# Kernel optimization log

Measured on AMD Instinct MI355X. Metric: run time of the kernel, lower is better.

Reference implementation:

```python
import jax, jax.numpy as jnp
import numpy as np
import math

EMBED_DIM = 256
NUM_HEADS = 8
FFN_DIM = 1024
EPS = 1e-5


def layer_norm(x, g, b):
    mu = jnp.mean(x, axis=-1, keepdims=True)
    var = jnp.var(x, axis=-1, keepdims=True)
    return (x - mu) / jnp.sqrt(var + EPS) * g + b


def setup_inputs() -> dict:
    key = jax.random.key(0)
    ks = jax.random.split(key, 10)
    B, L, D, F = 4, 2048, EMBED_DIM, FFN_DIM
    x = jax.random.normal(ks[0], (B, L, D), dtype=jnp.float32)
    mask = jnp.ones((B, L), dtype=jnp.int32)
    # FFN params (PyTorch Linear default-ish scale)
    W1 = jax.random.normal(ks[1], (D, F), dtype=jnp.float32) / np.sqrt(D)
    b1 = jnp.zeros((F,), dtype=jnp.float32)
    W2 = jax.random.normal(ks[2], (F, D), dtype=jnp.float32) / np.sqrt(F)
    b2 = jnp.zeros((D,), dtype=jnp.float32)
    g1 = jnp.ones((D,), dtype=jnp.float32)
    be1 = jnp.zeros((D,), dtype=jnp.float32)
    g2 = jnp.ones((D,), dtype=jnp.float32)
    be2 = jnp.zeros((D,), dtype=jnp.float32)
    return {"x": x, "mask": mask, "W1": W1, "b1": b1, "W2": W2, "b2": b2,
            "g1": g1, "be1": be1, "g2": g2, "be2": be2}


def quantum_attention(x, mask):
    B, L, D = x.shape
    H, dk = NUM_HEADS, D // NUM_HEADS
    xh = x.reshape(B, L, H, dk).transpose(0, 2, 1, 3)  # [B,H,L,dk]
    # per-token mean over batch and heads -> [L, dk]
    m = jnp.mean(xh, axis=(0, 1))
    # closed form of the single-qubit RX circuit: P(|1>) = sin^2(angle/2)
    dot = m @ m.T  # [L, L]
    ang = jnp.clip(dot, -math.pi, math.pi)
    scores = jnp.sin(ang * 0.5) ** 2  # [L, L], shared across B and H
    attn = jnp.broadcast_to(scores[None, None], (B, H, L, L))
    attn = jnp.where(mask[:, None, None, :] == 0, -1e9, attn)
    attn = jax.nn.softmax(attn, axis=-1)
    out = jnp.einsum('bhij,bhjd->bhid', attn, xh)  # values are xh itself
    return out.transpose(0, 2, 1, 3).reshape(B, L, D)


def reference(x, mask, W1, b1, W2, b2, g1, be1, g2, be2):
    attn_out = quantum_attention(x, mask)
    h = layer_norm(x + attn_out, g1, be1)
    ffn = jax.nn.relu(h @ W1 + b1) @ W2 + b2
    return layer_norm(h + ffn, g2, be2)
```

## Files before the change

### kernel.cpp

```cpp
#include <hip/hip_runtime.h>
#include <hip/hip_bf16.h>


#define B_ 4
#define L_ 2048
#define D_ 256
#define F_ 1024
#define PI_F 3.14159265358979323846f

typedef __bf16 bf16x8 __attribute__((ext_vector_type(8)));
typedef float floatx4 __attribute__((ext_vector_type(4)));
typedef unsigned short ushortx4 __attribute__((ext_vector_type(4)));
typedef unsigned short ushortx8 __attribute__((ext_vector_type(8)));

#define WAIT_VM(n) asm volatile("s_waitcnt vmcnt(" #n ")" ::: "memory")
#define WAIT_LGKM() asm volatile("s_waitcnt lgkmcnt(0)" ::: "memory")
#define SCHED0() __builtin_amdgcn_sched_barrier(0)
#define BARRIER() do { SCHED0(); __builtin_amdgcn_s_barrier(); SCHED0(); } while (0)

__device__ __forceinline__ unsigned short f2bf(float f) {
    unsigned int u = __float_as_uint(f);
    u = (u + 0x7FFFu + ((u >> 16) & 1u)) >> 16;
    return (unsigned short)u;
}
__device__ __forceinline__ float bf2f(unsigned short u) {
    union { unsigned int i; float f; } v; v.i = ((unsigned int)u) << 16; return v.f;
}

__device__ __forceinline__ void async_cp16(unsigned short* lds, const unsigned short* g) {
    __builtin_amdgcn_global_load_lds(
        (const __attribute__((address_space(1))) unsigned int*)g,
        (__attribute__((address_space(3))) unsigned int*)lds, 16, 0, 0);
}

__global__ __launch_bounds__(256) void k_prep(const float* __restrict__ x,
                                              const float* __restrict__ W1,
                                              const float* __restrict__ W2,
                                              const int* __restrict__ mask,
                                              unsigned short* __restrict__ mb,
                                              unsigned short* __restrict__ XmT,
                                              unsigned short* __restrict__ W1T,
                                              unsigned short* __restrict__ W2T) {
    __shared__ float ldsT[32 * 65];
    __shared__ float msk[64];
    int r = blockIdx.x, t = threadIdx.x;
    if (r >= 1280) {
        if (r < 1536) {
            int idx = (r - 1280) * 256 + t;
            int l = idx >> 5, k = idx & 31;
            float s = 0.f;
#pragma unroll
            for (int b = 0; b < B_; b++) {
                const float* xp = x + ((size_t)(b * L_ + l)) * D_ + k;
#pragma unroll
                for (int h = 0; h < 8; h++) s += xp[h * 32];
            }
            mb[idx] = f2bf(s * (1.f / 32.f));
        } else {
#pragma unroll
            for (int c = 0; c < 32; c++) {
                int e = c * 256 + t;
                int b = e >> 11, j = e & (L_ - 1);
                XmT[(size_t)(1024 + b) * L_ + j] = mask[b * L_ + j] ? 0x3F80 : 0;
            }
        }
        return;
    }
    const float* in; unsigned short* outp; int R, C; const int* mrow = nullptr; size_t bo = 0;
    int rt, cb;
    if (r < 1024) {
        int z = r >> 8, rem = r & 255;
        rt = rem >> 3; cb = rem & 7;
        in = x; outp = XmT; R = L_; C = 256; bo = (size_t)z * R * C;
        mrow = mask + z * L_;
    } else if (r < 1152) {
        int rem = r - 1024; rt = rem >> 5; cb = rem & 31;
        in = W1; outp = W1T; R = 256; C = 1024;
    } else {
        int rem = r - 1152; rt = rem >> 3; cb = rem & 7;
        in = W2; outp = W2T; R = 1024; C = 256;
    }
    int r0 = rt * 64, c0 = cb * 32;
    if (mrow && t < 64) msk[t] = mrow[r0 + t] ? 1.f : 0.f;
#pragma unroll
    for (int k = 0; k < 2; k++) {
        int q = t + k * 256;
        int row = q >> 3, cq = q & 7;
        float4 v = *(const float4*)(in + bo + (size_t)(r0 + row) * C + c0 + cq * 4);
        ldsT[(cq * 4 + 0) * 65 + row] = v.x;
        ldsT[(cq * 4 + 1) * 65 + row] = v.y;
        ldsT[(cq * 4 + 2) * 65 + row] = v.z;
        ldsT[(cq * 4 + 3) * 65 + row] = v.w;
    }
    __syncthreads();
#pragma unroll
    for (int k = 0; k < 2; k++) {
        int q = t + k * 256;
        int c = q >> 4, rq = q & 15;
        float f0 = ldsT[c * 65 + rq * 4 + 0];
        float f1 = ldsT[c * 65 + rq * 4 + 1];
        float f2 = ldsT[c * 65 + rq * 4 + 2];
        float f3 = ldsT[c * 65 + rq * 4 + 3];
        if (mrow) {
            f0 *= msk[rq * 4 + 0];
            f1 *= msk[rq * 4 + 1];
            f2 *= msk[rq * 4 + 2];
            f3 *= msk[rq * 4 + 3];
        }
        ushortx4 o;
        o.x = f2bf(f0); o.y = f2bf(f1); o.z = f2bf(f2); o.w = f2bf(f3);
        *(ushortx4*)(outp + bo + (size_t)(c0 + c) * R + r0 + rq * 4) = o;
    }
}

__global__ __launch_bounds__(256) void k_scores_mfma(const unsigned short* __restrict__ mb,
                                                     unsigned short* __restrict__ E) {
    const int t = threadIdx.x, lane = t & 63, wid = t >> 6;
    const int wm = (wid >> 1) * 64, wn = (wid & 1) * 32;
    const int lr = lane & 15, lq = lane >> 4;
    int m0 = blockIdx.y * 128, n0 = blockIdx.x * 64;
    bf16x8 af[4], bfr[2];
#pragma unroll
    for (int i = 0; i < 4; i++)
        af[i] = *(const bf16x8*)(mb + (size_t)(m0 + wm + i * 16 + lr) * 32 + lq * 8);
#pragma unroll
    for (int j = 0; j < 2; j++)
        bfr[j] = *(const bf16x8*)(mb + (size_t)(n0 + wn + j * 16 + lr) * 32 + lq * 8);
    floatx4 acc[4][2];
#pragma unroll
    for (int i = 0; i < 4; i++)
#pragma unroll
        for (int j = 0; j < 2; j++) {
            acc[i][j] = (floatx4){0.f, 0.f, 0.f, 0.f};
            acc[i][j] = __builtin_amdgcn_mfma_f32_16x16x32_bf16(af[i], bfr[j], acc[i][j], 0, 0, 0);
        }
#pragma unroll
    for (int i = 0; i < 4; i++)
#pragma unroll
        for (int j = 0; j < 2; j++)
#pragma unroll
            for (int r = 0; r < 4; r++) {
                int row = m0 + wm + i * 16 + lq * 4 + r;
                int col = n0 + wn + j * 16 + lr;
                float d = fminf(fmaxf(acc[i][j][r], -PI_F), PI_F);
                float sn = __sinf(0.5f * d);
                E[(size_t)row * L_ + col] = f2bf(__expf(sn * sn));
            }
}

__global__ __launch_bounds__(512) void k_av(const unsigned short* __restrict__ E,
                                            const unsigned short* __restrict__ XmT,
                                            unsigned short* __restrict__ Cb,
                                            float* __restrict__ rs) {
    __shared__ __align__(16) unsigned short sbuf[3][64 * 64 + 64 * 64 + 16 * 64];
    const int t = threadIdx.x, lane = t & 63, wid = t >> 6;
    const int wm = (wid >> 1) * 16, wn = (wid & 1) * 32;
    const int lr = lane & 15, lq = lane >> 4;
    const int lrow = lane >> 3, lseg = lane & 7;

    int bid = blockIdx.x;
    int swz = (bid & 7) * 64 + (bid >> 3);
    int m0 = (swz >> 4) * 64, n0 = (swz & 15) * 64;
    const bool doMask = (n0 == 0);
    const bool maskw = doMask && ((wid & 1) == 0);
    const bool mload = doMask && (wid < 2);

    const unsigned short* Ag; int sAoff;
    {
        int rl = wid * 8 + lrow;
        Ag = E + (size_t)(m0 + rl) * L_ + ((lseg - rl) & 7) * 8;
        sAoff = (wid * 8) * 64;
    }
    const unsigned short* Bg; int sBoff;
    {
        int rl = wid * 8 + lrow;
        Bg = XmT + (size_t)(n0 + rl) * L_ + ((lseg - rl) & 7) * 8;
        sBoff = 4096 + (wid * 8) * 64;
    }
    const unsigned short* Mg; int sMoff;
    {
        int rl = wid * 8 + lrow;
        Mg = XmT + (size_t)(1024 + rl) * L_ + ((lseg - rl) & 7) * 8;
        sMoff = 8192 + (wid * 8) * 64;
    }

    const int aroff = (wm + lr) * 64, arot = lq + wm + lr;
    int broff[2], brot[2];
#pragma unroll
    for (int j = 0; j < 2; j++) { int br = wn + j * 16 + lr; broff[j] = 4096 + br * 64; brot[j] = lq + br; }
    const int mroff = 8192 + lr * 64, mrot = lq + lr;

    floatx4 acc[2], acc3;
#pragma unroll
    for (int j = 0; j < 2; j++) acc[j] = (floatx4){0.f, 0.f, 0.f, 0.f};
    acc3 = (floatx4){0.f, 0.f, 0.f, 0.f};

    auto stage = [&](unsigned short* base, int k0) {
        async_cp16(base + sAoff, Ag + k0);
        async_cp16(base + sBoff, Bg + k0);
        if (mload) async_cp16(base + sMoff, Mg + k0);
    };
    auto compute = [&](const unsigned short* base) {
#pragma unroll
        for (int s = 0; s < 2; s++) {
            bf16x8 af = *(const bf16x8*)(base + aroff + ((s * 4 + arot) & 7) * 8);
#pragma unroll
            for (int j = 0; j < 2; j++) {
                bf16x8 bfr = *(const bf16x8*)(base + broff[j] + ((s * 4 + brot[j]) & 7) * 8);
                acc[j] = __builtin_amdgcn_mfma_f32_16x16x32_bf16(af, bfr, acc[j], 0, 0, 0);
            }
            if (maskw) {
                bf16x8 bm = *(const bf16x8*)(base + mroff + ((s * 4 + mrot) & 7) * 8);
                acc3 = __builtin_amdgcn_mfma_f32_16x16x32_bf16(af, bm, acc3, 0, 0, 0);
            }
        }
    };

    unsigned short *p0 = sbuf[0], *p1 = sbuf[1], *p2 = sbuf[2];
    stage(p0, 0); stage(p1, 64); stage(p2, 128);
    if (mload) { WAIT_VM(6); } else { WAIT_VM(4); }
    BARRIER();
    for (int p = 0; p < 29; ++p) {
        compute(p0);
        BARRIER();
        stage(p0, (p + 3) << 6);
        if (mload) { WAIT_VM(6); } else { WAIT_VM(4); }
        BARRIER();
        unsigned short* tmp = p0; p0 = p1; p1 = p2; p2 = tmp;
    }
    compute(p0); BARRIER();
    if (mload) { WAIT_VM(3); } else { WAIT_VM(2); }
    BARRIER();
    compute(p1); BARRIER();
    WAIT_VM(0); BARRIER();
    compute(p2);

#pragma unroll
    for (int j = 0; j < 2; j++)
#pragma unroll
        for (int r = 0; r < 4; r++) {
            int row = m0 + wm + lq * 4 + r;
            int col = n0 + wn + j * 16 + lr;
            Cb[(size_t)row * 1024 + col] = f2bf(acc[j][r]);
        }
    if (maskw && lr < 4) {
#pragma unroll
        for (int r = 0; r < 4; r++) {
            int row = m0 + wm + lq * 4 + r;
            rs[(size_t)row * 4 + lr] = acc3[r];
        }
    }
}

__global__ __launch_bounds__(512, 1) void k_ffn(const float* __restrict__ x,
                                                const unsigned short* __restrict__ Cb,
                                                const float* __restrict__ rs,
                                                const unsigned short* __restrict__ W1T,
                                                const unsigned short* __restrict__ W2T,
                                                const float* __restrict__ b1,
                                                const float* __restrict__ b2,
                                                const float* __restrict__ g1, const float* __restrict__ be1,
                                                const float* __restrict__ g2, const float* __restrict__ be2,
                                                float* __restrict__ out) {
    __shared__ __align__(16) unsigned short hA[4 * 32 * 64];
    __shared__ __align__(16) unsigned short W1b[2][4 * 64 * 64];
    __shared__ __align__(16) unsigned short W2b[2][4 * 64 * 64];
    __shared__ __align__(16) unsigned short t1c[2][32 * 72];
    __shared__ float b1s[1024];
    __shared__ float red[4][32][2];

    const int t = threadIdx.x, lane = t & 63, wid = t >> 6;
    const bool isG1 = wid < 4;
    const int gw = wid & 3;
    const int lr = lane & 15, lq = lane >> 4;
    const int half = lane >> 5, l32 = lane & 31;
    const int lrow8 = lane >> 3, kk = lane & 7;
    const int m0 = blockIdx.x * 32;

    auto stageW1 = [&](unsigned short* buf, int fc) {
#pragma unroll
        for (int q = 0; q < 8; q++) {
            int kc = q >> 1, sub = q & 1;
            int fl = sub * 32 + gw * 8 + lrow8;
            const unsigned short* src = W1T + (size_t)(fc * 64 + fl) * 256 + kc * 64 + (((kk - fl) & 7) * 8);
            async_cp16(buf + kc * 4096 + sub * 2048 + gw * 512, src);
        }
    };
    auto stageW2 = [&](unsigned short* buf, int fc) {
#pragma unroll
        for (int q = 0; q < 8; q++) {
            int nc = q >> 1, sub = q & 1;
            int nl = sub * 32 + gw * 8 + lrow8;
            const unsigned short* src = W2T + (size_t)(nc * 64 + nl) * 1024 + fc * 64 + (((kk - nl) & 7) * 8);
            async_cp16(buf + nc * 4096 + sub * 2048 + gw * 512, src);
        }
    };

    if (isG1) { stageW1(W1b[0], 0); stageW1(W1b[1], 1); }
    else      { stageW2(W2b[0], 0); stageW2(W2b[1], 1); }

    b1s[t] = b1[t];
    b1s[512 + t] = b1[512 + t];
    float4 g1a = *(const float4*)(g1 + l32 * 8);
    float4 g1b = *(const float4*)(g1 + l32 * 8 + 4);
    float4 be1a = *(const float4*)(be1 + l32 * 8);
    float4 be1b = *(const float4*)(be1 + l32 * 8 + 4);

#pragma unroll
    for (int it = 0; it < 2; it++) {
        int tloc = wid * 4 + it * 2 + half;
        int tok = m0 + tloc;
        int bi = tok >> 11, ii = tok & (L_ - 1);
        float rsv = rs[(size_t)ii * 4 + bi];
        float4 xv0 = *(const float4*)(x + (size_t)tok * D_ + l32 * 8);
        float4 xv1 = *(const float4*)(x + (size_t)tok * D_ + l32 * 8 + 4);
        ushortx8 cv = *(const ushortx8*)(Cb + (size_t)ii * 1024 + bi * 256 + l32 * 8);
        float v[8];
        v[0] = xv0.x + bf2f(cv[0]) / rsv; v[1] = xv0.y + bf2f(cv[1]) / rsv;
        v[2] = xv0.z + bf2f(cv[2]) / rsv; v[3] = xv0.w + bf2f(cv[3]) / rsv;
        v[4] = xv1.x + bf2f(cv[4]) / rsv; v[5] = xv1.y + bf2f(cv[5]) / rsv;
        v[6] = xv1.z + bf2f(cv[6]) / rsv; v[7] = xv1.w + bf2f(cv[7]) / rsv;
        float s = 0.f, s2 = 0.f;
#pragma unroll
        for (int k = 0; k < 8; k++) { s += v[k]; s2 += v[k] * v[k]; }
#pragma unroll
        for (int o = 1; o < 32; o <<= 1) { s += __shfl_xor(s, o); s2 += __shfl_xor(s2, o); }
        float mu = s * (1.f / 256.f);
        float var = s2 * (1.f / 256.f) - mu * mu;
        float rq = rsqrtf(var + 1e-5f);
        union { bf16x8 v8; unsigned short u[8]; } hv;
        hv.u[0] = f2bf((v[0] - mu) * rq * g1a.x + be1a.x);
        hv.u[1] = f2bf((v[1] - mu) * rq * g1a.y + be1a.y);
        hv.u[2] = f2bf((v[2] - mu) * rq * g1a.z + be1a.z);
        hv.u[3] = f2bf((v[3] - mu) * rq * g1a.w + be1a.w);
        hv.u[4] = f2bf((v[4] - mu) * rq * g1b.x + be1b.x);
        hv.u[5] = f2bf((v[5] - mu) * rq * g1b.y + be1b.y);
        hv.u[6] = f2bf((v[6] - mu) * rq * g1b.z + be1b.z);
        hv.u[7] = f2bf((v[7] - mu) * rq * g1b.w + be1b.w);
        *(bf16x8*)(hA + (l32 >> 3) * 2048 + tloc * 64 + ((((l32 & 7) + tloc) & 7) * 8)) = hv.v8;
    }
    WAIT_VM(0); WAIT_LGKM(); BARRIER();

    bf16x8 haf[2][8];
    if (isG1) {
#pragma unroll
        for (int i = 0; i < 2; i++)
#pragma unroll
            for (int kc = 0; kc < 4; kc++)
#pragma unroll
                for (int s = 0; s < 2; s++) {
                    int row = i * 16 + lr;
                    haf[i][kc * 2 + s] = *(const bf16x8*)(hA + kc * 2048 + row * 64 + (((s * 4 + lq + row) & 7) * 8));
                }
    }

    floatx4 acc[2][4];
#pragma unroll
    for (int i = 0; i < 2; i++)
#pragma unroll
        for (int j = 0; j < 4; j++) acc[i][j] = (floatx4){0.f, 0.f, 0.f, 0.f};

    const int wcol = gw * 16 + lr;

#pragma unroll 1
    for (int cc = 0; cc <= 16; ++cc) {
        if (cc >= 15) { WAIT_VM(0); } else { WAIT_VM(8); }
        BARRIER();
        if (isG1) {
            if (cc < 16) {
                const unsigned short* w1cur = W1b[cc & 1];
                floatx4 a1[2] = { (floatx4){0.f,0.f,0.f,0.f}, (floatx4){0.f,0.f,0.f,0.f} };
#pragma unroll
                for (int kc = 0; kc < 4; kc++)
#pragma unroll
                    for (int s = 0; s < 2; s++) {
                        bf16x8 bfr = *(const bf16x8*)(w1cur + kc * 4096 + wcol * 64 + (((s * 4 + lq + wcol) & 7) * 8));
                        a1[0] = __builtin_amdgcn_mfma_f32_16x16x32_bf16(haf[0][kc * 2 + s], bfr, a1[0], 0, 0, 0);
                        a1[1] = __builtin_amdgcn_mfma_f32_16x16x32_bf16(haf[1][kc * 2 + s], bfr, a1[1], 0, 0, 0);
                    }
                float bv = b1s[cc * 64 + wcol];
                unsigned short* tc = t1c[cc & 1];
#pragma unroll
                for (int i = 0; i < 2; i++)
#pragma unroll
                    for (int r = 0; r < 4; r++)
                        tc[(i * 16 + lq * 4 + r) * 72 + wcol] = f2bf(fmaxf(a1[i][r] + bv, 0.f));
                WAIT_LGKM();
            }
        } else {
            if (cc >= 1) {
                int d = cc - 1;
                const unsigned short* w2cur = W2b[d & 1];
                const unsigned short* tc = t1c[d & 1];
#pragma unroll
                for (int s = 0; s < 2; s++) {
                    bf16x8 af0 = *(const bf16x8*)(tc + lr * 72 + s * 32 + lq * 8);
                    bf16x8 af1 = *(const bf16x8*)(tc + (16 + lr) * 72 + s * 32 + lq * 8);
#pragma unroll
                    for (int j = 0; j < 4; j++) {
                        int nl = j * 16 + lr;
                        bf16x8 bfr = *(const bf16x8*)(w2cur + gw * 4096 + nl * 64 + (((s * 4 + lq + nl) & 7) * 8));
                        acc[0][j] = __builtin_amdgcn_mfma_f32_16x16x32_bf16(af0, bfr, acc[0][j], 0, 0, 0);
                        acc[1][j] = __builtin_amdgcn_mfma_f32_16x16x32_bf16(af1, bfr, acc[1][j], 0, 0, 0);
                    }
                }
            }
        }
        BARRIER();
        if (isG1) {
            if (cc <= 13) stageW1(W1b[cc & 1], cc + 2);
        } else {
            if (cc >= 1 && cc <= 14) stageW2(W2b[(cc - 1) & 1], cc + 1);
        }
    }

    float psum[2][4], psq[2][4];
#pragma unroll
    for (int i = 0; i < 2; i++)
#pragma unroll
        for (int r = 0; r < 4; r++) { psum[i][r] = 0.f; psq[i][r] = 0.f; }
    if (!isG1) {
#pragma unroll
        for (int i = 0; i < 2; i++)
#pragma unroll
            for (int j = 0; j < 4; j++) {
                int col = gw * 64 + j * 16 + lr;
                float bv = b2[col];
                int kc = col >> 6, ks = (col >> 3) & 7, ke = col & 7;
#pragma unroll
                for (int r = 0; r < 4; r++) {
                    int row = i * 16 + lq * 4 + r;
                    float hres = bf2f(hA[kc * 2048 + row * 64 + (((ks + row) & 7) * 8) + ke]);
                    float v = acc[i][j][r] + bv + hres;
                    acc[i][j][r] = v;
                    psum[i][r] += v; psq[i][r] += v * v;
                }
            }
#pragma unroll
        for (int o = 1; o < 16; o <<= 1)
#pragma unroll
            for (int i = 0; i < 2; i++)
#pragma unroll
                for (int r = 0; r < 4; r++) { psum[i][r] += __shfl_xor(psum[i][r], o); psq[i][r] += __shfl_xor(psq[i][r], o); }
        if (lr == 0) {
#pragma unroll
            for (int i = 0; i < 2; i++)
#pragma unroll
                for (int r = 0; r < 4; r++) {
                    int lrow = i * 16 + lq * 4 + r;
                    red[gw][lrow][0] = psum[i][r];
                    red[gw][lrow][1] = psq[i][r];
                }
        }
    }
    __syncthreads();
    if (!isG1) {
#pragma unroll
        for (int i = 0; i < 2; i++)
#pragma unroll
            for (int r = 0; r < 4; r++) {
                int lrow = i * 16 + lq * 4 + r;
                float s  = red[0][lrow][0] + red[1][lrow][0] + red[2][lrow][0] + red[3][lrow][0];
                float s2 = red[0][lrow][1] + red[1][lrow][1] + red[2][lrow][1] + red[3][lrow][1];
                float mu = s * (1.f / 256.f);
                float var = s2 * (1.f / 256.f) - mu * mu;
                float rc = rsqrtf(var + 1e-5f);
                int row = m0 + lrow;
#pragma unroll
                for (int j = 0; j < 4; j++) {
                    int col = gw * 64 + j * 16 + lr;
                    out[(size_t)row * 256 + col] = (acc[i][j][r] - mu) * rc * g2[col] + be2[col];
                }
            }
    }
}

extern "C" void kernel_launch(void* const* d_in, const int* in_sizes, int n_in,
                              void* d_out, int out_size, void* d_ws, size_t ws_size,
                              hipStream_t stream) {
    const float* x   = (const float*)d_in[0];
    const int*  mask = (const int*)d_in[1];
    const float* W1  = (const float*)d_in[2];
    const float* b1  = (const float*)d_in[3];
    const float* W2  = (const float*)d_in[4];
    const float* b2  = (const float*)d_in[5];
    const float* g1  = (const float*)d_in[6];
    const float* be1 = (const float*)d_in[7];
    const float* g2  = (const float*)d_in[8];
    const float* be2 = (const float*)d_in[9];
    float* out = (float*)d_out;

    char* w = (char*)d_ws;
    unsigned short* mb_   = (unsigned short*)w;  w += 65536 * 2;
    unsigned short* E_    = (unsigned short*)w;  w += (size_t)L_ * L_ * 2;
    unsigned short* XmT_  = (unsigned short*)w;  w += (size_t)1088 * L_ * 2;
    unsigned short* W1T_  = (unsigned short*)w;  w += 262144 * 2;
    unsigned short* W2T_  = (unsigned short*)w;  w += 262144 * 2;
    unsigned short* Cb_   = (unsigned short*)w;  w += (size_t)L_ * 1024 * 2;
    float*          rs_   = (float*)w;           w += (size_t)L_ * 4 * 4;

    k_prep<<<1537, 256, 0, stream>>>(x, W1, W2, mask, mb_, XmT_, W1T_, W2T_);
    k_scores_mfma<<<dim3(32, 16), 256, 0, stream>>>(mb_, E_);
    k_av<<<512, 512, 0, stream>>>(E_, XmT_, Cb_, rs_);
    k_ffn<<<256, 512, 0, stream>>>(x, Cb_, rs_, W1T_, W2T_, b1, b2, g1, be1, g2, be2, out);
}
```

Before: 126.9 us.

## Switch k_av to double-buffered K=128 tiles instead of triple-buffered K=64

The attention-times-values kernel now stages 128-wide K slices into two LDS buffers instead of 64-wide slices into three. Each thread issues two async copies per matrix per stage, and compute runs four MFMA k-steps per tile with a 16-segment swizzle. This halves the number of barriers and loop iterations, but prefetch depth drops to a single tile ahead while LDS use grows.

```diff
diff --git a/kernel.cpp b/kernel.cpp
--- a/kernel.cpp
+++ b/kernel.cpp
@@ -152,11 +152,11 @@
                                             const unsigned short* __restrict__ XmT,
                                             unsigned short* __restrict__ Cb,
                                             float* __restrict__ rs) {
-    __shared__ __align__(16) unsigned short sbuf[3][64 * 64 + 64 * 64 + 16 * 64];
+    __shared__ __align__(16) unsigned short sbuf[2][(64 + 64 + 16) * 128];
     const int t = threadIdx.x, lane = t & 63, wid = t >> 6;
     const int wm = (wid >> 1) * 16, wn = (wid & 1) * 32;
     const int lr = lane & 15, lq = lane >> 4;
-    const int lrow = lane >> 3, lseg = lane & 7;
+    const int lrow4 = lane >> 4, lg = lane & 15;
 
     int bid = blockIdx.x;
     int swz = (bid & 7) * 64 + (bid >> 3);
@@ -165,30 +165,25 @@
     const bool maskw = doMask && ((wid & 1) == 0);
     const bool mload = doMask && (wid < 2);
 
-    const unsigned short* Ag; int sAoff;
-    {
-        int rl = wid * 8 + lrow;
-        Ag = E + (size_t)(m0 + rl) * L_ + ((lseg - rl) & 7) * 8;
-        sAoff = (wid * 8) * 64;
-    }
-    const unsigned short* Bg; int sBoff;
-    {
-        int rl = wid * 8 + lrow;
-        Bg = XmT + (size_t)(n0 + rl) * L_ + ((lseg - rl) & 7) * 8;
-        sBoff = 4096 + (wid * 8) * 64;
-    }
-    const unsigned short* Mg; int sMoff;
-    {
-        int rl = wid * 8 + lrow;
-        Mg = XmT + (size_t)(1024 + rl) * L_ + ((lseg - rl) & 7) * 8;
-        sMoff = 8192 + (wid * 8) * 64;
-    }
-
-    const int aroff = (wm + lr) * 64, arot = lq + wm + lr;
+    const unsigned short* Ag[2]; int sAoff[2];
+    const unsigned short* Bg[2]; int sBoff[2];
+    const unsigned short* Mg[2]; int sMoff[2];
+#pragma unroll
+    for (int q = 0; q < 2; q++) {
+        int rl = wid * 8 + q * 4 + lrow4;
+        Ag[q] = E + (size_t)(m0 + rl) * L_ + ((lg - rl) & 15) * 8;
+        sAoff[q] = (wid * 8 + q * 4) * 128;
+        Bg[q] = XmT + (size_t)(n0 + rl) * L_ + ((lg - rl) & 15) * 8;
+        sBoff[q] = 8192 + (wid * 8 + q * 4) * 128;
+        Mg[q] = XmT + (size_t)(1024 + rl) * L_ + ((lg - rl) & 15) * 8;
+        sMoff[q] = 16384 + (wid * 8 + q * 4) * 128;
+    }
+
+    const int aroff = (wm + lr) * 128, arot = lq + wm + lr;
     int broff[2], brot[2];
 #pragma unroll
-    for (int j = 0; j < 2; j++) { int br = wn + j * 16 + lr; broff[j] = 4096 + br * 64; brot[j] = lq + br; }
-    const int mroff = 8192 + lr * 64, mrot = lq + lr;
+    for (int j = 0; j < 2; j++) { int br = wn + j * 16 + lr; broff[j] = 8192 + br * 128; brot[j] = lq + br; }
+    const int mroff = 16384 + lr * 128, mrot = lq + lr;
 
     floatx4 acc[2], acc3;
 #pragma unroll
@@ -196,44 +191,48 @@
     acc3 = (floatx4){0.f, 0.f, 0.f, 0.f};
 
     auto stage = [&](unsigned short* base, int k0) {
-        async_cp16(base + sAoff, Ag + k0);
-        async_cp16(base + sBoff, Bg + k0);
-        if (mload) async_cp16(base + sMoff, Mg + k0);
+#pragma unroll
+        for (int q = 0; q < 2; q++) {
+            async_cp16(base + sAoff[q], Ag[q] + k0);
+            async_cp16(base + sBoff[q], Bg[q] + k0);
+        }
+        if (mload) {
+#pragma unroll
+            for (int q = 0; q < 2; q++) async_cp16(base + sMoff[q], Mg[q] + k0);
+        }
     };
     auto compute = [&](const unsigned short* base) {
 #pragma unroll
-        for (int s = 0; s < 2; s++) {
-            bf16x8 af = *(const bf16x8*)(base + aroff + ((s * 4 + arot) & 7) * 8);
+        for (int s = 0; s < 4; s++) {
+            bf16x8 af = *(const bf16x8*)(base + aroff + ((s * 4 + arot) & 15) * 8);
 #pragma unroll
             for (int j = 0; j < 2; j++) {
-                bf16x8 bfr = *(const bf16x8*)(base + broff[j] + ((s * 4 + brot[j]) & 7) * 8);
+                bf16x8 bfr = *(const bf16x8*)(base + broff[j] + ((s * 4 + brot[j]) & 15) * 8);
                 acc[j] = __builtin_amdgcn_mfma_f32_16x16x32_bf16(af, bfr, acc[j], 0, 0, 0);
             }
             if (maskw) {
-                bf16x8 bm = *(const bf16x8*)(base + mroff + ((s * 4 + mrot) & 7) * 8);
+                bf16x8 bm = *(const bf16x8*)(base + mroff + ((s * 4 + mrot) & 15) * 8);
                 acc3 = __builtin_amdgcn_mfma_f32_16x16x32_bf16(af, bm, acc3, 0, 0, 0);
             }
         }
     };
 
-    unsigned short *p0 = sbuf[0], *p1 = sbuf[1], *p2 = sbuf[2];
-    stage(p0, 0); stage(p1, 64); stage(p2, 128);
+    unsigned short *p0 = sbuf[0], *p1 = sbuf[1];
+    stage(p0, 0); stage(p1, 128);
     if (mload) { WAIT_VM(6); } else { WAIT_VM(4); }
     BARRIER();
-    for (int p = 0; p < 29; ++p) {
+    for (int p = 0; p < 14; ++p) {
         compute(p0);
         BARRIER();
-        stage(p0, (p + 3) << 6);
+        stage(p0, (p + 2) << 7);
         if (mload) { WAIT_VM(6); } else { WAIT_VM(4); }
         BARRIER();
-        unsigned short* tmp = p0; p0 = p1; p1 = p2; p2 = tmp;
-    }
-    compute(p0); BARRIER();
-    if (mload) { WAIT_VM(3); } else { WAIT_VM(2); }
+        unsigned short* tmp = p0; p0 = p1; p1 = tmp;
+    }
+    compute(p0);
     BARRIER();
-    compute(p1); BARRIER();
     WAIT_VM(0); BARRIER();
-    compute(p2);
+    compute(p1);
 
 #pragma unroll
     for (int j = 0; j < 2; j++)
```

Measured after the change: 130.1 us. 2.5% more time.
